# Performance work log

Measured on AMD Instinct MI355X. Metric: run time of the kernel, lower is better.

## Reference

```python
import jax, jax.numpy as jnp
import numpy as np

B, S, H, NH = 2, 2048, 2048, 16
HD = H // NH
SCALE = 1.0 / np.sqrt(HD).astype(np.float32)


def setup_inputs() -> dict:
    key = jax.random.key(0)
    ks = jax.random.split(key, 10)
    std = 1.0 / np.sqrt(H)
    return {
        "x": jax.random.normal(ks[0], (B, S, H), dtype=jnp.float32),
        "attention_mask": jnp.zeros((B, 1, 1, S), dtype=jnp.float32),
        "Wq": jax.random.normal(ks[1], (H, H), dtype=jnp.float32) * std,
        "bq": jnp.zeros((H,), dtype=jnp.float32),
        "Wk": jax.random.normal(ks[2], (H, H), dtype=jnp.float32) * std,
        "bk": jnp.zeros((H,), dtype=jnp.float32),
        "Wv": jax.random.normal(ks[3], (H, H), dtype=jnp.float32) * std,
        "bv": jnp.zeros((H,), dtype=jnp.float32),
        "Wo": jax.random.normal(ks[4], (H, H), dtype=jnp.float32) * std,
        "bo": jnp.zeros((H,), dtype=jnp.float32),
    }


def _heads(t):
    # [B,S,H] -> [B,NH,S,HD]
    return t.reshape(B, S, NH, HD).transpose(0, 2, 1, 3)


def reference(x, attention_mask, Wq, bq, Wk, bk, Wv, bv, Wo, bo):
    q = _heads(x @ Wq.T + bq)
    k = _heads(x @ Wk.T + bk)
    v = _heads(x @ Wv.T + bv)
    scores = jnp.einsum("bhqd,bhkd->bhqk", q, k) * SCALE + attention_mask
    probs = jax.nn.softmax(scores, axis=-1)
    ctx = jnp.einsum("bhqk,bhkd->bhqd", probs, v)
    ctx = ctx.transpose(0, 2, 1, 3).reshape(B, S, H)
    return ctx @ Wo.T + bo
```

## Files before the change

### kernel.cpp

```cpp
#include <hip/hip_runtime.h>
#include <cstdint>
#include <cstddef>

#define B_   2
#define S_   2048
#define H_   2048
#define NH_  16
#define HD_  128
#define MM_  (B_ * S_)
#define K_   H_
#define SCALE_F 0.08838834764831845f
#define LOG2E_F 1.4426950408889634f
#define QSCALE_F (SCALE_F * LOG2E_F)

typedef __bf16 bf16_t;
typedef __attribute__((ext_vector_type(8))) __bf16 bf16x8;
typedef __attribute__((ext_vector_type(4))) __bf16 bf16x4;
typedef __attribute__((ext_vector_type(4))) float  f32x4;
typedef __attribute__((ext_vector_type(4))) float  floatx4;

static __device__ __forceinline__ f32x4 mfma_16x16x32(bf16x8 a, bf16x8 b, f32x4 c) {
  return __builtin_amdgcn_mfma_f32_16x16x32_bf16(a, b, c, 0, 0, 0);
}

static __device__ __forceinline__ void gl2lds16(const bf16_t* g, bf16_t* l) {
  __builtin_amdgcn_global_load_lds(
      (const __attribute__((address_space(1))) void*)g,
      (__attribute__((address_space(3))) void*)l, 16, 0, 0);
}

static __device__ __forceinline__ float exp2_hw(float x) {
  float r;
  asm("v_exp_f32 %0, %1" : "=v"(r) : "v"(x));
  return r;
}

__global__ void cvt6_f32_bf16(const float* __restrict__ x,
                              const float* __restrict__ w0, const float* __restrict__ w1,
                              const float* __restrict__ w2, const float* __restrict__ w3,
                              bf16_t* xo, bf16_t* o0, bf16_t* o1, bf16_t* o2, bf16_t* o3,
                              int n8) {
  const int yy = blockIdx.y;
  const float* in;
  bf16_t* out;
  if (yy == 0)      { in = x;                      out = xo; }
  else if (yy == 1) { in = x + (size_t)H_ * H_;    out = xo + (size_t)H_ * H_; }
  else if (yy == 2) { in = w0; out = o0; }
  else if (yy == 3) { in = w1; out = o1; }
  else if (yy == 4) { in = w2; out = o2; }
  else              { in = w3; out = o3; }
  int i = blockIdx.x * blockDim.x + threadIdx.x;
  const int stride = gridDim.x * blockDim.x;
  for (; i < n8; i += stride) {
    const floatx4* p = (const floatx4*)(in + (size_t)i * 8);
    floatx4 a = p[0], b = p[1];
    bf16x8 o;
    o[0] = (bf16_t)a.x; o[1] = (bf16_t)a.y; o[2] = (bf16_t)a.z; o[3] = (bf16_t)a.w;
    o[4] = (bf16_t)b.x; o[5] = (bf16_t)b.y; o[6] = (bf16_t)b.z; o[7] = (bf16_t)b.w;
    *(bf16x8*)(out + (size_t)i * 8) = o;
  }
}

template <int MODE, int NCOLS>
__global__ __launch_bounds__(256) void gemm_bt(
    const bf16_t* __restrict__ A,
    const bf16_t* __restrict__ W0, const bf16_t* __restrict__ W1, const bf16_t* __restrict__ W2,
    const float* __restrict__ bias0, const float* __restrict__ bias1, const float* __restrict__ bias2,
    bf16_t* __restrict__ dq, bf16_t* __restrict__ dk, bf16_t* __restrict__ dv,
    float* __restrict__ outf)
{
  __shared__ __align__(16) bf16_t Ash[128 * 32];
  __shared__ __align__(16) bf16_t Bsh[128 * 32];

  const int t = threadIdx.x;
  const int lane = t & 63;
  const int wid  = t >> 6;
  const int wm = wid >> 1, wn = wid & 1;

  const int lin = blockIdx.x;
  const int xcd = lin & 7;
  const int loc = lin >> 3;
  const int sr  = loc >> 5;
  const int l   = loc & 31;
  const int r_  = xcd * (NCOLS / 8) + sr;
  const int tm  = (r_ & 3) * 8 + (l & 7);
  const int nc  = (r_ >> 2) * 4 + (l >> 3);
  const int bm  = tm * 128;

  int bn;
  int wsel = 0;
  const bf16_t* Bw;
  const float*  bias;
  bf16_t* dsth = nullptr;
  if constexpr (MODE == 0) {
    wsel = nc >> 4;
    bn   = (nc & 15) * 128;
    Bw   = (wsel == 0) ? W0 : ((wsel == 1) ? W1 : W2);
    bias = (wsel == 0) ? bias0 : ((wsel == 1) ? bias1 : bias2);
    dsth = (wsel == 0) ? dq : ((wsel == 1) ? dk : dv);
  } else {
    bn = nc * 128;
    Bw = W0; bias = bias0;
  }

  const bf16_t* gA = A  + (size_t)(bm + (t >> 2)) * K_ + (t & 3) * 8;
  const bf16_t* gB = Bw + (size_t)(bn + (t >> 2)) * K_ + (t & 3) * 8;
  bf16_t* lA = Ash + wid * 512;
  bf16_t* lB = Bsh + wid * 512;

  f32x4 acc[4][4] = {};

  #pragma unroll 1
  for (int k0 = 0; k0 < K_; k0 += 32) {
    gl2lds16(gA + k0,                    lA);
    gl2lds16(gA + k0 + (size_t)64 * K_,  lA + 2048);
    gl2lds16(gB + k0,                    lB);
    gl2lds16(gB + k0 + (size_t)64 * K_,  lB + 2048);
    __syncthreads();

    bf16x8 af[4], bfr[4];
    #pragma unroll
    for (int i = 0; i < 4; ++i) {
      af[i]  = *(const bf16x8*)&Ash[(wm * 64 + i * 16 + (lane & 15)) * 32 + (lane >> 4) * 8];
      bfr[i] = *(const bf16x8*)&Bsh[(wn * 64 + i * 16 + (lane & 15)) * 32 + (lane >> 4) * 8];
    }
    __builtin_amdgcn_s_setprio(1);
    #pragma unroll
    for (int i = 0; i < 4; ++i)
      #pragma unroll
      for (int j = 0; j < 4; ++j)
        acc[i][j] = mfma_16x16x32(af[i], bfr[j], acc[i][j]);
    __builtin_amdgcn_s_setprio(0);
    __syncthreads();
  }

  const int row0 = bm + wm * 64 + (lane >> 4) * 4;
  const int col0 = bn + wn * 64 + (lane & 15);
  #pragma unroll
  for (int j = 0; j < 4; ++j) {
    const int col = col0 + j * 16;
    const float bv = bias[col];
    #pragma unroll
    for (int i = 0; i < 4; ++i) {
      #pragma unroll
      for (int r = 0; r < 4; ++r) {
        const int row = row0 + i * 16 + r;
        float v = acc[i][j][r] + bv;
        if constexpr (MODE == 0) {
          const int ss = row & (S_ - 1);
          const int dd = col & (HD_ - 1);
          const size_t bh = (size_t)((row >> 11) * NH_ + (col >> 7));
          if (wsel == 0) v *= QSCALE_F;
          size_t idx;
          if (wsel == 2) {
            const size_t t1 = bh * 32 + (ss >> 6);
            const size_t t2 = t1 * 8 + (dd >> 4);
            const size_t t3 = t2 * 2 + ((ss >> 5) & 1);
            const size_t ln = (size_t)((dd & 15) | (((ss >> 3) & 3) << 4));
            idx = (t3 * 64 + ln) * 8 + (size_t)(ss & 7);
          } else {
            const size_t t1 = bh * 128 + (ss >> 4);
            const size_t t2 = t1 * 4 + (dd >> 5);
            const size_t ln = (size_t)((ss & 15) | (((dd >> 3) & 3) << 4));
            idx = (t2 * 64 + ln) * 8 + (size_t)(dd & 7);
          }
          dsth[idx] = (bf16_t)v;
        } else {
          outf[(size_t)row * H_ + col] = v;
        }
      }
    }
  }
}

#define KVB 64
#define NT_ (S_ / KVB)
#define TILE_E 8192

__global__ __launch_bounds__(128, 2) void attn_kernel(
    const bf16_t* __restrict__ Qf, const bf16_t* __restrict__ Kf,
    const bf16_t* __restrict__ Vf, const float* __restrict__ mask,
    bf16_t* __restrict__ ctx)
{
  __shared__ __align__(16) bf16_t Klds[TILE_E];
  __shared__ __align__(16) bf16_t Vlds[TILE_E];
  __shared__ __align__(16) bf16_t Plds[2][2048];

  const int t = threadIdx.x;
  const int lane = t & 63;
  const int wid  = t >> 6;
  const int g    = lane >> 4;

  const int orig = blockIdx.x;
  const int wg = (orig & 7) * 128 + (orig >> 3);
  const int qt = wg & 31;
  const int bh = wg >> 5;
  const int b  = bh >> 4;
  const int h  = bh & 15;
  const int q0 = qt * 64 + wid * 32;

  const bf16_t* Kh0 = Kf + (size_t)bh * (NT_ * TILE_E);
  const bf16_t* Vh0 = Vf + (size_t)bh * (NT_ * TILE_E);
  const float*  mg  = mask + (size_t)b * S_;

  const bf16_t* Qt = Qf + (((size_t)bh * 128 + (q0 >> 4)) * 4) * 512;
  bf16x8 qf[2][4];
  #pragma unroll
  for (int mh = 0; mh < 2; ++mh)
    #pragma unroll
    for (int ks = 0; ks < 4; ++ks)
      qf[mh][ks] = *(const bf16x8*)&Qt[((mh * 4 + ks) * 64 + lane) * 8];

  f32x4 acc[2][8] = {};
  float m_run[2] = {-INFINITY, -INFINITY};
  float l_run[2] = {0.0f, 0.0f};

  char* Pw = (char*)&Plds[wid][0];

  auto stage = [&](int it) {
    const bf16_t* Ksrc = Kh0 + (size_t)it * TILE_E;
    const bf16_t* Vsrc = Vh0 + (size_t)it * TILE_E;
    #pragma unroll
    for (int i = 0; i < 8; ++i) {
      const int base = (i * 128 + wid * 64) * 8;
      gl2lds16(Ksrc + base + lane * 8, &Klds[base]);
      gl2lds16(Vsrc + base + lane * 8, &Vlds[base]);
    }
  };

  #pragma unroll 1
  for (int it = 0; it < NT_; ++it) {
    stage(it);

    const int kv0 = it * KVB;
    floatx4 mv[4];
    #pragma unroll
    for (int ns = 0; ns < 4; ++ns)
      mv[ns] = *(const floatx4*)&mg[kv0 + ns * 16 + g * 4];

    __syncthreads();

    f32x4 sacc[2][4] = {};
    #pragma unroll
    for (int ns = 0; ns < 4; ++ns) {
      #pragma unroll
      for (int ks = 0; ks < 4; ++ks) {
        const bf16x8 kf = *(const bf16x8*)&Klds[((ns * 4 + ks) * 64 + lane) * 8];
        __builtin_amdgcn_s_setprio(1);
        sacc[0][ns] = mfma_16x16x32(kf, qf[0][ks], sacc[0][ns]);
        sacc[1][ns] = mfma_16x16x32(kf, qf[1][ks], sacc[1][ns]);
        __builtin_amdgcn_s_setprio(0);
      }
    }

    float tmax[2];
    #pragma unroll
    for (int mh = 0; mh < 2; ++mh) {
      float tm = -INFINITY;
      #pragma unroll
      for (int ns = 0; ns < 4; ++ns)
        #pragma unroll
        for (int r = 0; r < 4; ++r) {
          sacc[mh][ns][r] += mv[ns][r];
          tm = fmaxf(tm, sacc[mh][ns][r]);
        }
      tm = fmaxf(tm, __shfl_xor(tm, 16));
      tm = fmaxf(tm, __shfl_xor(tm, 32));
      tmax[mh] = tm;
    }

    const bool small = (tmax[0] <= m_run[0] + 8.0f) && (tmax[1] <= m_run[1] + 8.0f);
    if (!__all(small)) {
      #pragma unroll
      for (int mh = 0; mh < 2; ++mh) {
        const float mnew = fmaxf(m_run[mh], tmax[mh]);
        const float scl  = exp2_hw(m_run[mh] - mnew);
        m_run[mh] = mnew;
        l_run[mh] *= scl;
        #pragma unroll
        for (int ds = 0; ds < 8; ++ds)
          #pragma unroll
          for (int r = 0; r < 4; ++r)
            acc[mh][ds][r] *= scl;
      }
    }

    float rs[2] = {0.0f, 0.0f};
    #pragma unroll
    for (int mh = 0; mh < 2; ++mh) {
      #pragma unroll
      for (int ns = 0; ns < 4; ++ns) {
        bf16x4 pk;
        #pragma unroll
        for (int r = 0; r < 4; ++r) {
          const float p = exp2_hw(sacc[mh][ns][r] - m_run[mh]);
          rs[mh] += p;
          pk[r] = (bf16_t)p;
        }
        const int L = (lane & 15) | ((((ns & 1) << 1) | (g >> 1)) << 4);
        const int byte = mh * 2048 + ((ns >> 1) << 10) + L * 16 + (g & 1) * 8;
        *(bf16x4*)(Pw + byte) = pk;
      }
    }

    bf16x8 pf[2][2];
    #pragma unroll
    for (int mh = 0; mh < 2; ++mh)
      #pragma unroll
      for (int ks2 = 0; ks2 < 2; ++ks2)
        pf[mh][ks2] = *(const bf16x8*)(Pw + mh * 2048 + ks2 * 1024 + lane * 16);

    #pragma unroll
    for (int ds = 0; ds < 8; ++ds) {
      const bf16x8 vf0 = *(const bf16x8*)&Vlds[((ds * 2 + 0) * 64 + lane) * 8];
      const bf16x8 vf1 = *(const bf16x8*)&Vlds[((ds * 2 + 1) * 64 + lane) * 8];
      __builtin_amdgcn_s_setprio(1);
      #pragma unroll
      for (int mh = 0; mh < 2; ++mh) {
        acc[mh][ds] = mfma_16x16x32(vf0, pf[mh][0], acc[mh][ds]);
        acc[mh][ds] = mfma_16x16x32(vf1, pf[mh][1], acc[mh][ds]);
      }
      __builtin_amdgcn_s_setprio(0);
    }

    #pragma unroll
    for (int mh = 0; mh < 2; ++mh) {
      rs[mh] += __shfl_xor(rs[mh], 16);
      rs[mh] += __shfl_xor(rs[mh], 32);
      l_run[mh] += rs[mh];
    }

    __syncthreads();
  }

  #pragma unroll
  for (int mh = 0; mh < 2; ++mh) {
    const int q = q0 + mh * 16 + (lane & 15);
    const float inv = 1.0f / l_run[mh];
    #pragma unroll
    for (int ds = 0; ds < 8; ++ds) {
      bf16x4 o;
      #pragma unroll
      for (int r = 0; r < 4; ++r)
        o[r] = (bf16_t)(acc[mh][ds][r] * inv);
      *(bf16x4*)&ctx[((size_t)(b * S_ + q)) * H_ + h * HD_ + ds * 16 + g * 4] = o;
    }
  }
}

extern "C" void kernel_launch(void* const* d_in, const int* in_sizes, int n_in,
                              void* d_out, int out_size, void* d_ws, size_t ws_size,
                              hipStream_t stream) {
  (void)in_sizes; (void)n_in; (void)out_size; (void)ws_size;
  const float* x    = (const float*)d_in[0];
  const float* mask = (const float*)d_in[1];
  const float* Wq   = (const float*)d_in[2];
  const float* bq   = (const float*)d_in[3];
  const float* Wk   = (const float*)d_in[4];
  const float* bk   = (const float*)d_in[5];
  const float* Wv   = (const float*)d_in[6];
  const float* bv   = (const float*)d_in[7];
  const float* Wo   = (const float*)d_in[8];
  const float* bo   = (const float*)d_in[9];
  float* out = (float*)d_out;

  const size_t nX = (size_t)MM_ * H_;
  const size_t nW = (size_t)H_ * H_;

  bf16_t* xbf = (bf16_t*)d_ws;
  bf16_t* wqb = xbf + nX;
  bf16_t* wkb = wqb + nW;
  bf16_t* wvb = wkb + nW;
  bf16_t* wob = wvb + nW;
  bf16_t* qf  = wob + nW;
  bf16_t* kf  = qf + nX;
  bf16_t* vf  = kf + nX;
  bf16_t* cxb = vf + nX;

  cvt6_f32_bf16<<<dim3(512, 6), 256, 0, stream>>>(
      x, Wq, Wk, Wv, Wo, xbf, wqb, wkb, wvb, wob, (int)(nW / 8));

  gemm_bt<0, 48><<<32 * 48, 256, 0, stream>>>(
      xbf, wqb, wkb, wvb, bq, bk, bv, qf, kf, vf, nullptr);

  attn_kernel<<<1024, 128, 0, stream>>>(qf, kf, vf, mask, cxb);

  gemm_bt<1, 16><<<32 * 16, 256, 0, stream>>>(
      cxb, wob, nullptr, nullptr, bo, nullptr, nullptr, nullptr, nullptr, nullptr, out);
}
```

Baseline: 308.9 us.

## Double GEMM K-tile to 64 with XOR-swizzled LDS layout

The projection GEMM now loads 64-wide K slices per iteration instead of 32, which halves the number of barrier pairs per tile and doubles MFMA work between syncs. The LDS layout uses an XOR swizzle on 16-byte column groups by row to avoid bank conflicts on the wider rows. This doubles LDS usage per block, which may reduce occupancy.

```diff
diff --git a/kernel.cpp b/kernel.cpp
--- a/kernel.cpp
+++ b/kernel.cpp
@@ -69,8 +69,8 @@
     bf16_t* __restrict__ dq, bf16_t* __restrict__ dk, bf16_t* __restrict__ dv,
     float* __restrict__ outf)
 {
-  __shared__ __align__(16) bf16_t Ash[128 * 32];
-  __shared__ __align__(16) bf16_t Bsh[128 * 32];
+  __shared__ __align__(16) bf16_t Ash[128 * 64];
+  __shared__ __align__(16) bf16_t Bsh[128 * 64];
 
   const int t = threadIdx.x;
   const int lane = t & 63;
@@ -103,33 +103,45 @@
     Bw = W0; bias = bias0;
   }
 
-  const bf16_t* gA = A  + (size_t)(bm + (t >> 2)) * K_ + (t & 3) * 8;
-  const bf16_t* gB = Bw + (size_t)(bn + (t >> 2)) * K_ + (t & 3) * 8;
-  bf16_t* lA = Ash + wid * 512;
-  bf16_t* lB = Bsh + wid * 512;
+  const bf16_t* gA = A  + (size_t)bm * K_;
+  const bf16_t* gB = Bw + (size_t)bn * K_;
 
   f32x4 acc[4][4] = {};
 
   #pragma unroll 1
-  for (int k0 = 0; k0 < K_; k0 += 32) {
-    gl2lds16(gA + k0,                    lA);
-    gl2lds16(gA + k0 + (size_t)64 * K_,  lA + 2048);
-    gl2lds16(gB + k0,                    lB);
-    gl2lds16(gB + k0 + (size_t)64 * K_,  lB + 2048);
+  for (int k0 = 0; k0 < K_; k0 += 64) {
+    #pragma unroll
+    for (int j = 0; j < 4; ++j) {
+      const int c = j * 256 + t;
+      const int R = c >> 3;
+      const int g = (c & 7) ^ (R & 7);
+      bf16_t* la = Ash + (j * 256 + wid * 64) * 8;
+      bf16_t* lb = Bsh + (j * 256 + wid * 64) * 8;
+      gl2lds16(gA + (size_t)R * K_ + k0 + g * 8, la);
+      gl2lds16(gB + (size_t)R * K_ + k0 + g * 8, lb);
+    }
     __syncthreads();
 
-    bf16x8 af[4], bfr[4];
-    #pragma unroll
-    for (int i = 0; i < 4; ++i) {
-      af[i]  = *(const bf16x8*)&Ash[(wm * 64 + i * 16 + (lane & 15)) * 32 + (lane >> 4) * 8];
-      bfr[i] = *(const bf16x8*)&Bsh[(wn * 64 + i * 16 + (lane & 15)) * 32 + (lane >> 4) * 8];
-    }
+    bf16x8 af[4][2], bfr[4][2];
+    #pragma unroll
+    for (int i = 0; i < 4; ++i)
+      #pragma unroll
+      for (int kk = 0; kk < 2; ++kk) {
+        const int Ra = wm * 64 + i * 16 + (lane & 15);
+        const int ca = (kk * 4 + (lane >> 4)) ^ (Ra & 7);
+        af[i][kk] = *(const bf16x8*)&Ash[Ra * 64 + ca * 8];
+        const int Rb = wn * 64 + i * 16 + (lane & 15);
+        const int cb = (kk * 4 + (lane >> 4)) ^ (Rb & 7);
+        bfr[i][kk] = *(const bf16x8*)&Bsh[Rb * 64 + cb * 8];
+      }
     __builtin_amdgcn_s_setprio(1);
     #pragma unroll
-    for (int i = 0; i < 4; ++i)
-      #pragma unroll
-      for (int j = 0; j < 4; ++j)
-        acc[i][j] = mfma_16x16x32(af[i], bfr[j], acc[i][j]);
+    for (int kk = 0; kk < 2; ++kk)
+      #pragma unroll
+      for (int i = 0; i < 4; ++i)
+        #pragma unroll
+        for (int j2 = 0; j2 < 4; ++j2)
+          acc[i][j2] = mfma_16x16x32(af[i][kk], bfr[j2][kk], acc[i][j2]);
     __builtin_amdgcn_s_setprio(0);
     __syncthreads();
   }
@@ -137,15 +149,15 @@
   const int row0 = bm + wm * 64 + (lane >> 4) * 4;
   const int col0 = bn + wn * 64 + (lane & 15);
   #pragma unroll
-  for (int j = 0; j < 4; ++j) {
-    const int col = col0 + j * 16;
+  for (int j2 = 0; j2 < 4; ++j2) {
+    const int col = col0 + j2 * 16;
     const float bv = bias[col];
     #pragma unroll
     for (int i = 0; i < 4; ++i) {
       #pragma unroll
       for (int r = 0; r < 4; ++r) {
         const int row = row0 + i * 16 + r;
-        float v = acc[i][j][r] + bv;
+        float v = acc[i][j2][r] + bv;
         if constexpr (MODE == 0) {
           const int ss = row & (S_ - 1);
           const int dd = col & (HD_ - 1);
```

After: 280.5 us (median of 2 runs). -9.2%, faster.
